# Kernel optimization log

Hardware: AMD Instinct MI355X
Metric: run time of the kernel (lower is better)

The kernel has to match this reference:

```python
import jax, jax.numpy as jnp
import numpy as np

D_MODEL = 1024
NUM_HEADS = 16
D_K = D_MODEL // NUM_HEADS


def setup_inputs() -> dict:
    key = jax.random.key(0)
    ks = jax.random.split(key, 9)
    B, S = 4, 2048
    scale = 1.0 / np.sqrt(D_MODEL)
    return {
        "hidden_states": jax.random.normal(ks[0], (B, S, D_MODEL), dtype=jnp.float32),
        "Wq": jax.random.normal(ks[1], (D_MODEL, D_MODEL), dtype=jnp.float32) * scale,
        "bq": jax.random.normal(ks[2], (D_MODEL,), dtype=jnp.float32) * 0.02,
        "Wk": jax.random.normal(ks[3], (D_MODEL, D_MODEL), dtype=jnp.float32) * scale,
        "bk": jax.random.normal(ks[4], (D_MODEL,), dtype=jnp.float32) * 0.02,
        "Wv": jax.random.normal(ks[5], (D_MODEL, D_MODEL), dtype=jnp.float32) * scale,
        "bv": jax.random.normal(ks[6], (D_MODEL,), dtype=jnp.float32) * 0.02,
        "Wout": jax.random.normal(ks[7], (D_MODEL, D_MODEL), dtype=jnp.float32) * scale,
        "bout": jax.random.normal(ks[8], (D_MODEL,), dtype=jnp.float32) * 0.02,
    }


def _split_heads(x):
    # [B, S, D] -> [B, H, S, d_k]
    B, S, _ = x.shape
    return x.reshape(B, S, NUM_HEADS, D_K).transpose(0, 2, 1, 3)


def reference(hidden_states, Wq, bq, Wk, bk, Wv, bv, Wout, bout):
    # torch nn.Linear convention: y = x @ W.T + b
    q = _split_heads(hidden_states @ Wq.T + bq)
    k = _split_heads(hidden_states @ Wk.T + bk)
    v = _split_heads(hidden_states @ Wv.T + bv)
    # scaled dot-product attention (no mask, matching attention_mask=None)
    scores = jnp.einsum("bhqd,bhkd->bhqk", q, k) / jnp.sqrt(jnp.float32(D_K))
    attn = jax.nn.softmax(scores, axis=-1)
    ctx = jnp.einsum("bhqk,bhkd->bhqd", attn, v)
    # concatenate heads: [B, H, S, d_k] -> [B, S, D]
    B, H, S, dk = ctx.shape
    ctx = ctx.transpose(0, 2, 1, 3).reshape(B, S, H * dk)
    return ctx @ Wout.T + bout
```

## Files before the change

### kernel.cpp

```cpp
#include <hip/hip_runtime.h>
#include <hip/hip_bf16.h>
#include <stdint.h>

#define DEV_INLINE __device__ __forceinline__

typedef __attribute__((ext_vector_type(4))) float f32x4;
typedef __attribute__((ext_vector_type(16))) float f32x16;
typedef __attribute__((ext_vector_type(8))) short short8;

static constexpr int S_LEN = 2048;
static constexpr int DM = 1024;
static constexpr int NH = 16;
static constexpr int DK = 64;
static constexpr int BATCH = 4;
static constexpr int M_TOT = BATCH * S_LEN;

#define QSCALE 0.18033688011112042f

DEV_INLINE unsigned short bf_round(float x) {
  unsigned u = __builtin_bit_cast(unsigned, x);
  u += 0x7fffu + ((u >> 16) & 1u);
  return (unsigned short)(u >> 16);
}

struct CvtArgs {
  const float* in[5];
  unsigned short* out[5];
};
__global__ __launch_bounds__(256) void cvt_all(CvtArgs a) {
  int bid = blockIdx.x;
  int which, base;
  if (bid < 4096) { which = 0; base = bid; }
  else { int r = bid - 4096; which = 1 + (r >> 9); base = r & 511; }
  const float* __restrict__ in = a.in[which];
  unsigned short* __restrict__ out = a.out[which];
  long i = ((long)base * 256 + threadIdx.x) * 8;
  float4 va = *reinterpret_cast<const float4*>(in + i);
  float4 vb = *reinterpret_cast<const float4*>(in + i + 4);
  union { unsigned short u[8]; uint4 v; } pk;
  pk.u[0] = bf_round(va.x); pk.u[1] = bf_round(va.y);
  pk.u[2] = bf_round(va.z); pk.u[3] = bf_round(va.w);
  pk.u[4] = bf_round(vb.x); pk.u[5] = bf_round(vb.y);
  pk.u[6] = bf_round(vb.z); pk.u[7] = bf_round(vb.w);
  *reinterpret_cast<uint4*>(out + i) = pk.v;
}

DEV_INLINE void gload_lds16(const unsigned short* g, unsigned short* l) {
  __builtin_amdgcn_global_load_lds(
      (const __attribute__((address_space(1))) unsigned int*)g,
      (__attribute__((address_space(3))) unsigned int*)l,
      16, 0, 0);
}

struct QkvArgs {
  const unsigned short* W[3];
  const float* bias[3];
  unsigned short* out[3];
};
__global__ __launch_bounds__(256) void gemm_qkv(const unsigned short* __restrict__ A,
                                                QkvArgs args) {
  constexpr int K = DM;
  __shared__ unsigned short lA[128 * 32];
  __shared__ unsigned short lB[128 * 32];
  const int tid = threadIdx.x;
  const int wave = tid >> 6, lane = tid & 63;
  const int wm = wave >> 1, wn = wave & 1;
  const int g = lane >> 4, c = lane & 15;
  const int bm = blockIdx.x, bn = blockIdx.y, z = blockIdx.z;

  const unsigned short* __restrict__ W = args.W[z];
  const float* __restrict__ bias = args.bias[z];
  unsigned short* __restrict__ outp = args.out[z];

  const int srow = lane >> 2;
  const int scol = (lane & 3) * 8;

  f32x4 acc[4][4] = {};

  const unsigned short* Abase = A + (long)(bm * 128) * K;
  const unsigned short* Wbase = W + (long)(bn * 128) * K;

  for (int k0 = 0; k0 < K; k0 += 32) {
    __syncthreads();
#pragma unroll
    for (int i = 0; i < 2; ++i) {
      const int row = i * 64 + wave * 16;
      gload_lds16(Abase + (long)(row + srow) * K + k0 + scol, lA + row * 32);
      gload_lds16(Wbase + (long)(row + srow) * K + k0 + scol, lB + row * 32);
    }
    __syncthreads();

    short8 af[4], bf[4];
#pragma unroll
    for (int mi = 0; mi < 4; ++mi)
      af[mi] = *reinterpret_cast<const short8*>(&lA[(wm * 64 + mi * 16 + c) * 32 + g * 8]);
#pragma unroll
    for (int ni = 0; ni < 4; ++ni)
      bf[ni] = *reinterpret_cast<const short8*>(&lB[(wn * 64 + ni * 16 + c) * 32 + g * 8]);
#pragma unroll
    for (int mi = 0; mi < 4; ++mi)
#pragma unroll
      for (int ni = 0; ni < 4; ++ni)
        acc[mi][ni] =
            __builtin_amdgcn_mfma_f32_16x16x32_bf16(af[mi], bf[ni], acc[mi][ni], 0, 0, 0);
  }

#pragma unroll
  for (int mi = 0; mi < 4; ++mi) {
#pragma unroll
    for (int ni = 0; ni < 4; ++ni) {
      const int mg0 = bm * 128 + wm * 64 + mi * 16 + g * 4;
      const int ng = bn * 128 + wn * 64 + ni * 16 + c;
      const float bv = bias[ng];
#pragma unroll
      for (int r = 0; r < 4; ++r) {
        const int m = mg0 + r;
        float v = acc[mi][ni][r] + bv;
        if (z == 0) v *= QSCALE;
        const int b_ = m >> 11, s_ = m & 2047, h_ = ng >> 6, d_ = ng & 63;
        if (z < 2) {
          outp[((long)(b_ * NH + h_) * S_LEN + s_) * DK + d_] = bf_round(v);
        } else {
          outp[((long)(b_ * NH + h_) * DK + d_) * S_LEN + s_] = bf_round(v);
        }
      }
    }
  }
}

__global__ __launch_bounds__(256) void gemm_out(const unsigned short* __restrict__ A,
                                                const unsigned short* __restrict__ W,
                                                const float* __restrict__ bias,
                                                float* __restrict__ outp) {
  constexpr int K = DM, N = DM;
  __shared__ unsigned short lA[128 * 32];
  __shared__ unsigned short lB[128 * 32];
  const int tid = threadIdx.x;
  const int wave = tid >> 6, lane = tid & 63;
  const int wm = wave >> 1, wn = wave & 1;
  const int g = lane >> 4, c = lane & 15;
  const int bm = blockIdx.x, bn = blockIdx.y;

  const int srow = lane >> 2;
  const int scol = (lane & 3) * 8;

  f32x4 acc[4][4] = {};

  const unsigned short* Abase = A + (long)(bm * 128) * K;
  const unsigned short* Wbase = W + (long)(bn * 128) * K;

  for (int k0 = 0; k0 < K; k0 += 32) {
    __syncthreads();
#pragma unroll
    for (int i = 0; i < 2; ++i) {
      const int row = i * 64 + wave * 16;
      gload_lds16(Abase + (long)(row + srow) * K + k0 + scol, lA + row * 32);
      gload_lds16(Wbase + (long)(row + srow) * K + k0 + scol, lB + row * 32);
    }
    __syncthreads();

    short8 af[4], bf[4];
#pragma unroll
    for (int mi = 0; mi < 4; ++mi)
      af[mi] = *reinterpret_cast<const short8*>(&lA[(wm * 64 + mi * 16 + c) * 32 + g * 8]);
#pragma unroll
    for (int ni = 0; ni < 4; ++ni)
      bf[ni] = *reinterpret_cast<const short8*>(&lB[(wn * 64 + ni * 16 + c) * 32 + g * 8]);
#pragma unroll
    for (int mi = 0; mi < 4; ++mi)
#pragma unroll
      for (int ni = 0; ni < 4; ++ni)
        acc[mi][ni] =
            __builtin_amdgcn_mfma_f32_16x16x32_bf16(af[mi], bf[ni], acc[mi][ni], 0, 0, 0);
  }

#pragma unroll
  for (int mi = 0; mi < 4; ++mi) {
#pragma unroll
    for (int ni = 0; ni < 4; ++ni) {
      const int mg0 = bm * 128 + wm * 64 + mi * 16 + g * 4;
      const int ng = bn * 128 + wn * 64 + ni * 16 + c;
      const float bv = bias[ng];
#pragma unroll
      for (int r = 0; r < 4; ++r)
        outp[(long)(mg0 + r) * N + ng] = acc[mi][ni][r] + bv;
    }
  }
}

__global__ __launch_bounds__(256) void attn_kernel(const unsigned short* __restrict__ Q,
                                                   const unsigned short* __restrict__ Kb,
                                                   const unsigned short* __restrict__ Vt,
                                                   unsigned short* __restrict__ ctx) {
  __shared__ unsigned short kbuf[2][64 * 64];
  __shared__ unsigned short vbuf[2][64 * 64];
  const int tid = threadIdx.x, wave = tid >> 6, lane = tid & 63;
  const int q = lane & 31;
  const int h = lane >> 5;
  const int bid = blockIdx.x;
  const int swz = (bid & 7) * 128 + (bid >> 3);
  const int hd = swz >> 4, qb = swz & 15;
  const int q0 = qb * 128 + wave * 32;

  const unsigned short* Qh = Q + (long)hd * S_LEN * DK;
  const char* KhB = (const char*)(Kb + (long)hd * S_LEN * DK);
  const char* VhB = (const char*)(Vt + (long)hd * DK * S_LEN);

  const int srow_in = lane >> 3;
  const int scolb = ((lane & 7) * 16) ^ (srow_in << 4);

  auto ldsrd = [&](const unsigned short* buf, int row, int colbyte) -> short8 {
    return *reinterpret_cast<const short8*>(
        reinterpret_cast<const char*>(buf) + row * 128 + (colbyte ^ ((row & 7) << 4)));
  };

  auto stage = [&](int b, int kv0) {
#pragma unroll
    for (int r = 0; r < 2; ++r) {
      const int rowbase = (wave * 2 + r) * 8;
      const int row = rowbase + srow_in;
      gload_lds16((const unsigned short*)(KhB + (long)(kv0 + row) * 128 + scolb),
                  &kbuf[b][rowbase * 64]);
      gload_lds16((const unsigned short*)(VhB + (long)row * (S_LEN * 2) + kv0 * 2 + scolb),
                  &vbuf[b][rowbase * 64]);
    }
  };

  short8 qf[4];
#pragma unroll
  for (int d0 = 0; d0 < 4; ++d0)
    qf[d0] = *reinterpret_cast<const short8*>(&Qh[(long)(q0 + q) * DK + d0 * 16 + h * 8]);

  f32x16 cacc0 = {}, cacc1 = {};
  float mrun = -1e30f, lrun = 0.0f;

  stage(0, 0);
  __syncthreads();

  int cur = 0;
  for (int t = 0; t < S_LEN / 64; ++t) {
    if (t + 1 < S_LEN / 64) stage(cur ^ 1, (t + 1) * 64);

    const unsigned short* kb = kbuf[cur];
    const unsigned short* vb = vbuf[cur];

    short8 kfA[4], kfB[4];
#pragma unroll
    for (int d0 = 0; d0 < 4; ++d0) {
      kfA[d0] = ldsrd(kb, q, d0 * 32 + h * 16);
      kfB[d0] = ldsrd(kb, 32 + q, d0 * 32 + h * 16);
    }
    __builtin_amdgcn_s_setprio(1);
    f32x16 stA = {}, stB = {};
#pragma unroll
    for (int d0 = 0; d0 < 4; ++d0) {
      stA = __builtin_amdgcn_mfma_f32_32x32x16_bf16(kfA[d0], qf[d0], stA, 0, 0, 0);
      stB = __builtin_amdgcn_mfma_f32_32x32x16_bf16(kfB[d0], qf[d0], stB, 0, 0, 0);
    }
    __builtin_amdgcn_s_setprio(0);

    float t16[16];
#pragma unroll
    for (int r = 0; r < 16; ++r) t16[r] = fmaxf(stA[r], stB[r]);
#pragma unroll
    for (int r = 0; r < 8; ++r) t16[r] = fmaxf(t16[r], t16[r + 8]);
#pragma unroll
    for (int r = 0; r < 4; ++r) t16[r] = fmaxf(t16[r], t16[r + 4]);
    const float pml = fmaxf(fmaxf(t16[0], t16[1]), fmaxf(t16[2], t16[3]));

    if (__any(pml > mrun + 8.0f)) {
      const float pm = fmaxf(pml, __shfl_xor(pml, 32));
      const float mnew = fmaxf(mrun, pm);
      const float alpha = __builtin_amdgcn_exp2f(mrun - mnew);
      cacc0 *= alpha;
      cacc1 *= alpha;
      lrun *= alpha;
      mrun = mnew;
    }

#pragma unroll
    for (int r = 0; r < 16; ++r) {
      stA[r] = __builtin_amdgcn_exp2f(stA[r] - mrun);
      stB[r] = __builtin_amdgcn_exp2f(stB[r] - mrun);
    }
    float s16[16];
#pragma unroll
    for (int r = 0; r < 16; ++r) s16[r] = stA[r] + stB[r];
#pragma unroll
    for (int r = 0; r < 8; ++r) s16[r] = s16[r] + s16[r + 8];
#pragma unroll
    for (int r = 0; r < 4; ++r) s16[r] = s16[r] + s16[r + 4];
    lrun += (s16[0] + s16[1]) + (s16[2] + s16[3]);

    unsigned pAA[4], pAB[4], pBA[4], pBB[4];
#pragma unroll
    for (int rq = 0; rq < 4; ++rq) {
      asm("v_cvt_pk_bf16_f32 %0, %1, %2" : "=v"(pAA[rq]) : "v"(stA[4 * rq]), "v"(stA[4 * rq + 1]));
      asm("v_cvt_pk_bf16_f32 %0, %1, %2" : "=v"(pAB[rq]) : "v"(stA[4 * rq + 2]), "v"(stA[4 * rq + 3]));
      asm("v_cvt_pk_bf16_f32 %0, %1, %2" : "=v"(pBA[rq]) : "v"(stB[4 * rq]), "v"(stB[4 * rq + 1]));
      asm("v_cvt_pk_bf16_f32 %0, %1, %2" : "=v"(pBB[rq]) : "v"(stB[4 * rq + 2]), "v"(stB[4 * rq + 3]));
    }

    unsigned rA[4], rB[4];
#pragma unroll
    for (int s = 0; s < 4; ++s) {
      const unsigned a0 = (s < 2 ? pAA : pBA)[2 * (s & 1)];
      const unsigned a1 = (s < 2 ? pAA : pBA)[2 * (s & 1) + 1];
      const unsigned b0 = (s < 2 ? pAB : pBB)[2 * (s & 1)];
      const unsigned b1 = (s < 2 ? pAB : pBB)[2 * (s & 1) + 1];
      rA[s] = (unsigned)__shfl_xor((int)(h ? a0 : a1), 32);
      rB[s] = (unsigned)__shfl_xor((int)(h ? b0 : b1), 32);
    }
    short8 vf0[4], vf1[4];
#pragma unroll
    for (int s = 0; s < 4; ++s) {
      vf0[s] = ldsrd(vb, q, s * 32 + h * 16);
      vf1[s] = ldsrd(vb, 32 + q, s * 32 + h * 16);
    }
    __builtin_amdgcn_s_setprio(1);
#pragma unroll
    for (int s = 0; s < 4; ++s) {
      const unsigned a0 = (s < 2 ? pAA : pBA)[2 * (s & 1)];
      const unsigned a1 = (s < 2 ? pAA : pBA)[2 * (s & 1) + 1];
      const unsigned b0 = (s < 2 ? pAB : pBB)[2 * (s & 1)];
      const unsigned b1 = (s < 2 ? pAB : pBB)[2 * (s & 1) + 1];
      union { unsigned w[4]; short8 v; } pf;
      pf.w[0] = h ? rA[s] : a0;
      pf.w[1] = h ? rB[s] : b0;
      pf.w[2] = h ? a1 : rA[s];
      pf.w[3] = h ? b1 : rB[s];
      cacc0 = __builtin_amdgcn_mfma_f32_32x32x16_bf16(vf0[s], pf.v, cacc0, 0, 0, 0);
      cacc1 = __builtin_amdgcn_mfma_f32_32x32x16_bf16(vf1[s], pf.v, cacc1, 0, 0, 0);
    }
    __builtin_amdgcn_s_setprio(0);

    __syncthreads();
    cur ^= 1;
  }

  lrun += __shfl_xor(lrun, 32);
  const float inv = 1.0f / lrun;
  const int b_ = hd >> 4, h_ = hd & 15;
  const long row = ((long)b_ * S_LEN + q0 + q) * DM + h_ * DK;
#pragma unroll
  for (int rq = 0; rq < 4; ++rq) {
    ushort4 w0, w1;
    w0.x = bf_round(cacc0[4 * rq + 0] * inv);
    w0.y = bf_round(cacc0[4 * rq + 1] * inv);
    w0.z = bf_round(cacc0[4 * rq + 2] * inv);
    w0.w = bf_round(cacc0[4 * rq + 3] * inv);
    w1.x = bf_round(cacc1[4 * rq + 0] * inv);
    w1.y = bf_round(cacc1[4 * rq + 1] * inv);
    w1.z = bf_round(cacc1[4 * rq + 2] * inv);
    w1.w = bf_round(cacc1[4 * rq + 3] * inv);
    *reinterpret_cast<ushort4*>(&ctx[row + 8 * rq + 4 * h]) = w0;
    *reinterpret_cast<ushort4*>(&ctx[row + 32 + 8 * rq + 4 * h]) = w1;
  }
}

extern "C" void kernel_launch(void* const* d_in, const int* in_sizes, int n_in,
                              void* d_out, int out_size, void* d_ws, size_t ws_size,
                              hipStream_t stream) {
  const float* X  = (const float*)d_in[0];
  const float* Wq = (const float*)d_in[1];
  const float* bq = (const float*)d_in[2];
  const float* Wk = (const float*)d_in[3];
  const float* bk = (const float*)d_in[4];
  const float* Wv = (const float*)d_in[5];
  const float* bv = (const float*)d_in[6];
  const float* Wo = (const float*)d_in[7];
  const float* bo = (const float*)d_in[8];

  char* ws = (char*)d_ws;
  const long MB = 1l << 20;
  unsigned short* Xbf = (unsigned short*)(ws + 0 * MB);
  unsigned short* Ctx = Xbf;
  unsigned short* Wqb = (unsigned short*)(ws + 16 * MB);
  unsigned short* Wkb = (unsigned short*)(ws + 18 * MB);
  unsigned short* Wvb = (unsigned short*)(ws + 20 * MB);
  unsigned short* Wob = (unsigned short*)(ws + 22 * MB);
  unsigned short* Qb  = (unsigned short*)(ws + 24 * MB);
  unsigned short* Kbf = (unsigned short*)(ws + 40 * MB);
  unsigned short* Vtb = (unsigned short*)(ws + 56 * MB);

  CvtArgs ca;
  ca.in[0] = X;  ca.out[0] = Xbf;
  ca.in[1] = Wq; ca.out[1] = Wqb;
  ca.in[2] = Wk; ca.out[2] = Wkb;
  ca.in[3] = Wv; ca.out[3] = Wvb;
  ca.in[4] = Wo; ca.out[4] = Wob;
  cvt_all<<<4096 + 4 * 512, 256, 0, stream>>>(ca);

  QkvArgs qa;
  qa.W[0] = Wqb; qa.bias[0] = bq; qa.out[0] = Qb;
  qa.W[1] = Wkb; qa.bias[1] = bk; qa.out[1] = Kbf;
  qa.W[2] = Wvb; qa.bias[2] = bv; qa.out[2] = Vtb;
  gemm_qkv<<<dim3(M_TOT / 128, DM / 128, 3), 256, 0, stream>>>(Xbf, qa);

  attn_kernel<<<dim3(1024), 256, 0, stream>>>(Qb, Kbf, Vtb, Ctx);

  gemm_out<<<dim3(M_TOT / 128, DM / 128), 256, 0, stream>>>(Ctx, Wob, bo, (float*)d_out);
}
```

Baseline: 227.7 us.

## Process two 32-row query tiles per wave in attention to reuse K/V fragments

Each wave now handles 64 query rows instead of 32, so every block covers 256 queries and the grid shrinks from 1024 to 512 blocks. K and V fragments read from LDS are reused across two independent query tiles, halving LDS reads and global K/V staging per query. The cost is roughly doubled accumulator and score register pressure, which may lower occupancy, and the smaller grid may leave compute units underused (512 blocks on a 256-CU device).

Measured after the change: 257.5 us. +13.1%, slower.

```diff
diff --git a/kernel.cpp b/kernel.cpp
--- a/kernel.cpp
+++ b/kernel.cpp
@@ -198,9 +198,9 @@
   const int q = lane & 31;
   const int h = lane >> 5;
   const int bid = blockIdx.x;
-  const int swz = (bid & 7) * 128 + (bid >> 3);
-  const int hd = swz >> 4, qb = swz & 15;
-  const int q0 = qb * 128 + wave * 32;
+  const int swz = (bid & 7) * 64 + (bid >> 3);
+  const int hd = swz >> 3, qb = swz & 7;
+  const int q0 = qb * 256 + wave * 64;
 
   const unsigned short* Qh = Q + (long)hd * S_LEN * DK;
   const char* KhB = (const char*)(Kb + (long)hd * S_LEN * DK);
@@ -226,13 +226,16 @@
     }
   };
 
-  short8 qf[4];
-#pragma unroll
-  for (int d0 = 0; d0 < 4; ++d0)
-    qf[d0] = *reinterpret_cast<const short8*>(&Qh[(long)(q0 + q) * DK + d0 * 16 + h * 8]);
-
-  f32x16 cacc0 = {}, cacc1 = {};
-  float mrun = -1e30f, lrun = 0.0f;
+  short8 qf0[4], qf1[4];
+#pragma unroll
+  for (int d0 = 0; d0 < 4; ++d0) {
+    qf0[d0] = *reinterpret_cast<const short8*>(&Qh[(long)(q0 + q) * DK + d0 * 16 + h * 8]);
+    qf1[d0] = *reinterpret_cast<const short8*>(&Qh[(long)(q0 + 32 + q) * DK + d0 * 16 + h * 8]);
+  }
+
+  f32x16 c00 = {}, c01 = {};
+  f32x16 c10 = {}, c11 = {};
+  float m0 = -1e30f, l0 = 0.0f, m1 = -1e30f, l1 = 0.0f;
 
   stage(0, 0);
   __syncthreads();
@@ -251,65 +254,82 @@
       kfB[d0] = ldsrd(kb, 32 + q, d0 * 32 + h * 16);
     }
     __builtin_amdgcn_s_setprio(1);
-    f32x16 stA = {}, stB = {};
+    f32x16 sA0 = {}, sB0 = {}, sA1 = {}, sB1 = {};
 #pragma unroll
     for (int d0 = 0; d0 < 4; ++d0) {
-      stA = __builtin_amdgcn_mfma_f32_32x32x16_bf16(kfA[d0], qf[d0], stA, 0, 0, 0);
-      stB = __builtin_amdgcn_mfma_f32_32x32x16_bf16(kfB[d0], qf[d0], stB, 0, 0, 0);
+      sA0 = __builtin_amdgcn_mfma_f32_32x32x16_bf16(kfA[d0], qf0[d0], sA0, 0, 0, 0);
+      sB0 = __builtin_amdgcn_mfma_f32_32x32x16_bf16(kfB[d0], qf0[d0], sB0, 0, 0, 0);
+      sA1 = __builtin_amdgcn_mfma_f32_32x32x16_bf16(kfA[d0], qf1[d0], sA1, 0, 0, 0);
+      sB1 = __builtin_amdgcn_mfma_f32_32x32x16_bf16(kfB[d0], qf1[d0], sB1, 0, 0, 0);
     }
     __builtin_amdgcn_s_setprio(0);
 
-    float t16[16];
-#pragma unroll
-    for (int r = 0; r < 16; ++r) t16[r] = fmaxf(stA[r], stB[r]);
-#pragma unroll
-    for (int r = 0; r < 8; ++r) t16[r] = fmaxf(t16[r], t16[r + 8]);
-#pragma unroll
-    for (int r = 0; r < 4; ++r) t16[r] = fmaxf(t16[r], t16[r + 4]);
-    const float pml = fmaxf(fmaxf(t16[0], t16[1]), fmaxf(t16[2], t16[3]));
-
-    if (__any(pml > mrun + 8.0f)) {
-      const float pm = fmaxf(pml, __shfl_xor(pml, 32));
-      const float mnew = fmaxf(mrun, pm);
-      const float alpha = __builtin_amdgcn_exp2f(mrun - mnew);
-      cacc0 *= alpha;
-      cacc1 *= alpha;
-      lrun *= alpha;
-      mrun = mnew;
+    float t0[16], t1[16];
+#pragma unroll
+    for (int r = 0; r < 16; ++r) { t0[r] = fmaxf(sA0[r], sB0[r]); t1[r] = fmaxf(sA1[r], sB1[r]); }
+#pragma unroll
+    for (int r = 0; r < 8; ++r) { t0[r] = fmaxf(t0[r], t0[r + 8]); t1[r] = fmaxf(t1[r], t1[r + 8]); }
+#pragma unroll
+    for (int r = 0; r < 4; ++r) { t0[r] = fmaxf(t0[r], t0[r + 4]); t1[r] = fmaxf(t1[r], t1[r + 4]); }
+    const float pml0 = fmaxf(fmaxf(t0[0], t0[1]), fmaxf(t0[2], t0[3]));
+    const float pml1 = fmaxf(fmaxf(t1[0], t1[1]), fmaxf(t1[2], t1[3]));
+
+    if (__any(fmaxf(pml0 - m0, pml1 - m1) > 8.0f)) {
+      const float pm0 = fmaxf(pml0, __shfl_xor(pml0, 32));
+      const float pm1 = fmaxf(pml1, __shfl_xor(pml1, 32));
+      const float mn0 = fmaxf(m0, pm0), mn1 = fmaxf(m1, pm1);
+      const float a0 = __builtin_amdgcn_exp2f(m0 - mn0);
+      const float a1 = __builtin_amdgcn_exp2f(m1 - mn1);
+      c00 *= a0; c01 *= a0; l0 *= a0; m0 = mn0;
+      c10 *= a1; c11 *= a1; l1 *= a1; m1 = mn1;
     }
 
 #pragma unroll
     for (int r = 0; r < 16; ++r) {
-      stA[r] = __builtin_amdgcn_exp2f(stA[r] - mrun);
-      stB[r] = __builtin_amdgcn_exp2f(stB[r] - mrun);
-    }
-    float s16[16];
-#pragma unroll
-    for (int r = 0; r < 16; ++r) s16[r] = stA[r] + stB[r];
-#pragma unroll
-    for (int r = 0; r < 8; ++r) s16[r] = s16[r] + s16[r + 8];
-#pragma unroll
-    for (int r = 0; r < 4; ++r) s16[r] = s16[r] + s16[r + 4];
-    lrun += (s16[0] + s16[1]) + (s16[2] + s16[3]);
-
-    unsigned pAA[4], pAB[4], pBA[4], pBB[4];
+      sA0[r] = __builtin_amdgcn_exp2f(sA0[r] - m0);
+      sB0[r] = __builtin_amdgcn_exp2f(sB0[r] - m0);
+      sA1[r] = __builtin_amdgcn_exp2f(sA1[r] - m1);
+      sB1[r] = __builtin_amdgcn_exp2f(sB1[r] - m1);
+    }
+    float u0[16], u1[16];
+#pragma unroll
+    for (int r = 0; r < 16; ++r) { u0[r] = sA0[r] + sB0[r]; u1[r] = sA1[r] + sB1[r]; }
+#pragma unroll
+    for (int r = 0; r < 8; ++r) { u0[r] += u0[r + 8]; u1[r] += u1[r + 8]; }
+#pragma unroll
+    for (int r = 0; r < 4; ++r) { u0[r] += u0[r + 4]; u1[r] += u1[r + 4]; }
+    l0 += (u0[0] + u0[1]) + (u0[2] + u0[3]);
+    l1 += (u1[0] + u1[1]) + (u1[2] + u1[3]);
+
+    unsigned p0AA[4], p0AB[4], p0BA[4], p0BB[4];
+    unsigned p1AA[4], p1AB[4], p1BA[4], p1BB[4];
 #pragma unroll
     for (int rq = 0; rq < 4; ++rq) {
-      asm("v_cvt_pk_bf16_f32 %0, %1, %2" : "=v"(pAA[rq]) : "v"(stA[4 * rq]), "v"(stA[4 * rq + 1]));
-      asm("v_cvt_pk_bf16_f32 %0, %1, %2" : "=v"(pAB[rq]) : "v"(stA[4 * rq + 2]), "v"(stA[4 * rq + 3]));
-      asm("v_cvt_pk_bf16_f32 %0, %1, %2" : "=v"(pBA[rq]) : "v"(stB[4 * rq]), "v"(stB[4 * rq + 1]));
-      asm("v_cvt_pk_bf16_f32 %0, %1, %2" : "=v"(pBB[rq]) : "v"(stB[4 * rq + 2]), "v"(stB[4 * rq + 3]));
-    }
-
-    unsigned rA[4], rB[4];
+      asm("v_cvt_pk_bf16_f32 %0, %1, %2" : "=v"(p0AA[rq]) : "v"(sA0[4 * rq]), "v"(sA0[4 * rq + 1]));
+      asm("v_cvt_pk_bf16_f32 %0, %1, %2" : "=v"(p0AB[rq]) : "v"(sA0[4 * rq + 2]), "v"(sA0[4 * rq + 3]));
+      asm("v_cvt_pk_bf16_f32 %0, %1, %2" : "=v"(p0BA[rq]) : "v"(sB0[4 * rq]), "v"(sB0[4 * rq + 1]));
+      asm("v_cvt_pk_bf16_f32 %0, %1, %2" : "=v"(p0BB[rq]) : "v"(sB0[4 * rq + 2]), "v"(sB0[4 * rq + 3]));
+      asm("v_cvt_pk_bf16_f32 %0, %1, %2" : "=v"(p1AA[rq]) : "v"(sA1[4 * rq]), "v"(sA1[4 * rq + 1]));
+      asm("v_cvt_pk_bf16_f32 %0, %1, %2" : "=v"(p1AB[rq]) : "v"(sA1[4 * rq + 2]), "v"(sA1[4 * rq + 3]));
+      asm("v_cvt_pk_bf16_f32 %0, %1, %2" : "=v"(p1BA[rq]) : "v"(sB1[4 * rq]), "v"(sB1[4 * rq + 1]));
+      asm("v_cvt_pk_bf16_f32 %0, %1, %2" : "=v"(p1BB[rq]) : "v"(sB1[4 * rq + 2]), "v"(sB1[4 * rq + 3]));
+    }
+
+    unsigned r0A[4], r0B[4], r1A[4], r1B[4];
 #pragma unroll
     for (int s = 0; s < 4; ++s) {
-      const unsigned a0 = (s < 2 ? pAA : pBA)[2 * (s & 1)];
-      const unsigned a1 = (s < 2 ? pAA : pBA)[2 * (s & 1) + 1];
-      const unsigned b0 = (s < 2 ? pAB : pBB)[2 * (s & 1)];
-      const unsigned b1 = (s < 2 ? pAB : pBB)[2 * (s & 1) + 1];
-      rA[s] = (unsigned)__shfl_xor((int)(h ? a0 : a1), 32);
-      rB[s] = (unsigned)__shfl_xor((int)(h ? b0 : b1), 32);
+      const unsigned a00 = (s < 2 ? p0AA : p0BA)[2 * (s & 1)];
+      const unsigned a01 = (s < 2 ? p0AA : p0BA)[2 * (s & 1) + 1];
+      const unsigned b00 = (s < 2 ? p0AB : p0BB)[2 * (s & 1)];
+      const unsigned b01 = (s < 2 ? p0AB : p0BB)[2 * (s & 1) + 1];
+      r0A[s] = (unsigned)__shfl_xor((int)(h ? a00 : a01), 32);
+      r0B[s] = (unsigned)__shfl_xor((int)(h ? b00 : b01), 32);
+      const unsigned a10 = (s < 2 ? p1AA : p1BA)[2 * (s & 1)];
+      const unsigned a11 = (s < 2 ? p1AA : p1BA)[2 * (s & 1) + 1];
+      const unsigned b10 = (s < 2 ? p1AB : p1BB)[2 * (s & 1)];
+      const unsigned b11 = (s < 2 ? p1AB : p1BB)[2 * (s & 1) + 1];
+      r1A[s] = (unsigned)__shfl_xor((int)(h ? a10 : a11), 32);
+      r1B[s] = (unsigned)__shfl_xor((int)(h ? b10 : b11), 32);
     }
     short8 vf0[4], vf1[4];
 #pragma unroll
@@ -320,17 +340,28 @@
     __builtin_amdgcn_s_setprio(1);
 #pragma unroll
     for (int s = 0; s < 4; ++s) {
-      const unsigned a0 = (s < 2 ? pAA : pBA)[2 * (s & 1)];
-      const unsigned a1 = (s < 2 ? pAA : pBA)[2 * (s & 1) + 1];
-      const unsigned b0 = (s < 2 ? pAB : pBB)[2 * (s & 1)];
-      const unsigned b1 = (s < 2 ? pAB : pBB)[2 * (s & 1) + 1];
-      union { unsigned w[4]; short8 v; } pf;
-      pf.w[0] = h ? rA[s] : a0;
-      pf.w[1] = h ? rB[s] : b0;
-      pf.w[2] = h ? a1 : rA[s];
-      pf.w[3] = h ? b1 : rB[s];
-      cacc0 = __builtin_amdgcn_mfma_f32_32x32x16_bf16(vf0[s], pf.v, cacc0, 0, 0, 0);
-      cacc1 = __builtin_amdgcn_mfma_f32_32x32x16_bf16(vf1[s], pf.v, cacc1, 0, 0, 0);
+      const unsigned a00 = (s < 2 ? p0AA : p0BA)[2 * (s & 1)];
+      const unsigned a01 = (s < 2 ? p0AA : p0BA)[2 * (s & 1) + 1];
+      const unsigned b00 = (s < 2 ? p0AB : p0BB)[2 * (s & 1)];
+      const unsigned b01 = (s < 2 ? p0AB : p0BB)[2 * (s & 1) + 1];
+      union { unsigned w[4]; short8 v; } pf0;
+      pf0.w[0] = h ? r0A[s] : a00;
+      pf0.w[1] = h ? r0B[s] : b00;
+      pf0.w[2] = h ? a01 : r0A[s];
+      pf0.w[3] = h ? b01 : r0B[s];
+      c00 = __builtin_amdgcn_mfma_f32_32x32x16_bf16(vf0[s], pf0.v, c00, 0, 0, 0);
+      c01 = __builtin_amdgcn_mfma_f32_32x32x16_bf16(vf1[s], pf0.v, c01, 0, 0, 0);
+      const unsigned a10 = (s < 2 ? p1AA : p1BA)[2 * (s & 1)];
+      const unsigned a11 = (s < 2 ? p1AA : p1BA)[2 * (s & 1) + 1];
+      const unsigned b10 = (s < 2 ? p1AB : p1BB)[2 * (s & 1)];
+      const unsigned b11 = (s < 2 ? p1AB : p1BB)[2 * (s & 1) + 1];
+      union { unsigned w[4]; short8 v; } pf1;
+      pf1.w[0] = h ? r1A[s] : a10;
+      pf1.w[1] = h ? r1B[s] : b10;
+      pf1.w[2] = h ? a11 : r1A[s];
+      pf1.w[3] = h ? b11 : r1B[s];
+      c10 = __builtin_amdgcn_mfma_f32_32x32x16_bf16(vf0[s], pf1.v, c10, 0, 0, 0);
+      c11 = __builtin_amdgcn_mfma_f32_32x32x16_bf16(vf1[s], pf1.v, c11, 0, 0, 0);
     }
     __builtin_amdgcn_s_setprio(0);
 
@@ -338,23 +369,35 @@
     cur ^= 1;
   }
 
-  lrun += __shfl_xor(lrun, 32);
-  const float inv = 1.0f / lrun;
+  l0 += __shfl_xor(l0, 32);
+  l1 += __shfl_xor(l1, 32);
+  const float inv0 = 1.0f / l0, inv1 = 1.0f / l1;
   const int b_ = hd >> 4, h_ = hd & 15;
-  const long row = ((long)b_ * S_LEN + q0 + q) * DM + h_ * DK;
+  const long row0 = ((long)b_ * S_LEN + q0 + q) * DM + h_ * DK;
+  const long row1 = ((long)b_ * S_LEN + q0 + 32 + q) * DM + h_ * DK;
 #pragma unroll
   for (int rq = 0; rq < 4; ++rq) {
-    ushort4 w0, w1;
-    w0.x = bf_round(cacc0[4 * rq + 0] * inv);
-    w0.y = bf_round(cacc0[4 * rq + 1] * inv);
-    w0.z = bf_round(cacc0[4 * rq + 2] * inv);
-    w0.w = bf_round(cacc0[4 * rq + 3] * inv);
-    w1.x = bf_round(cacc1[4 * rq + 0] * inv);
-    w1.y = bf_round(cacc1[4 * rq + 1] * inv);
-    w1.z = bf_round(cacc1[4 * rq + 2] * inv);
-    w1.w = bf_round(cacc1[4 * rq + 3] * inv);
-    *reinterpret_cast<ushort4*>(&ctx[row + 8 * rq + 4 * h]) = w0;
-    *reinterpret_cast<ushort4*>(&ctx[row + 32 + 8 * rq + 4 * h]) = w1;
+    ushort4 w0, w1, w2, w3;
+    w0.x = bf_round(c00[4 * rq + 0] * inv0);
+    w0.y = bf_round(c00[4 * rq + 1] * inv0);
+    w0.z = bf_round(c00[4 * rq + 2] * inv0);
+    w0.w = bf_round(c00[4 * rq + 3] * inv0);
+    w1.x = bf_round(c01[4 * rq + 0] * inv0);
+    w1.y = bf_round(c01[4 * rq + 1] * inv0);
+    w1.z = bf_round(c01[4 * rq + 2] * inv0);
+    w1.w = bf_round(c01[4 * rq + 3] * inv0);
+    w2.x = bf_round(c10[4 * rq + 0] * inv1);
+    w2.y = bf_round(c10[4 * rq + 1] * inv1);
+    w2.z = bf_round(c10[4 * rq + 2] * inv1);
+    w2.w = bf_round(c10[4 * rq + 3] * inv1);
+    w3.x = bf_round(c11[4 * rq + 0] * inv1);
+    w3.y = bf_round(c11[4 * rq + 1] * inv1);
+    w3.z = bf_round(c11[4 * rq + 2] * inv1);
+    w3.w = bf_round(c11[4 * rq + 3] * inv1);
+    *reinterpret_cast<ushort4*>(&ctx[row0 + 8 * rq + 4 * h]) = w0;
+    *reinterpret_cast<ushort4*>(&ctx[row0 + 32 + 8 * rq + 4 * h]) = w1;
+    *reinterpret_cast<ushort4*>(&ctx[row1 + 8 * rq + 4 * h]) = w2;
+    *reinterpret_cast<ushort4*>(&ctx[row1 + 32 + 8 * rq + 4 * h]) = w3;
   }
 }
 
@@ -397,7 +440,7 @@
   qa.W[2] = Wvb; qa.bias[2] = bv; qa.out[2] = Vtb;
   gemm_qkv<<<dim3(M_TOT / 128, DM / 128, 3), 256, 0, stream>>>(Xbf, qa);
 
-  attn_kernel<<<dim3(1024), 256, 0, stream>>>(Qb, Kbf, Vtb, Ctx);
+  attn_kernel<<<dim3(512), 256, 0, stream>>>(Qb, Kbf, Vtb, Ctx);
 
   gemm_out<<<dim3(M_TOT / 128, DM / 128), 256, 0, stream>>>(Ctx, Wob, bo, (float*)d_out);
 }
```

## Stage 128-key tiles per barrier and compute softmax row sums via MFMA

Applied to the files above, without the earlier changes.

The KV loop now stages two 64-row K/V sub-tiles per double-buffer slot, which halves the number of __syncthreads barriers and loads more data per prefetch. LDS use doubles to 64KB. The per-row softmax denominator is no longer a VALU reduction tree over fp32 probabilities. It is accumulated by an extra MFMA against a ones vector, using the bf16-rounded probabilities, which moves that work onto the matrix cores. The cost is 50% more MFMAs in the PV stage, possible occupancy loss from the larger LDS footprint, and a denominator computed from rounded values.

Result: no change. 226.5 us (-0.5%).

```diff
diff --git a/kernel.cpp b/kernel.cpp
--- a/kernel.cpp
+++ b/kernel.cpp
@@ -192,8 +192,8 @@
                                                    const unsigned short* __restrict__ Kb,
                                                    const unsigned short* __restrict__ Vt,
                                                    unsigned short* __restrict__ ctx) {
-  __shared__ unsigned short kbuf[2][64 * 64];
-  __shared__ unsigned short vbuf[2][64 * 64];
+  __shared__ unsigned short kbuf[2][2][64 * 64];
+  __shared__ unsigned short vbuf[2][2][64 * 64];
   const int tid = threadIdx.x, wave = tid >> 6, lane = tid & 63;
   const int q = lane & 31;
   const int h = lane >> 5;
@@ -216,13 +216,17 @@
 
   auto stage = [&](int b, int kv0) {
 #pragma unroll
-    for (int r = 0; r < 2; ++r) {
-      const int rowbase = (wave * 2 + r) * 8;
-      const int row = rowbase + srow_in;
-      gload_lds16((const unsigned short*)(KhB + (long)(kv0 + row) * 128 + scolb),
-                  &kbuf[b][rowbase * 64]);
-      gload_lds16((const unsigned short*)(VhB + (long)row * (S_LEN * 2) + kv0 * 2 + scolb),
-                  &vbuf[b][rowbase * 64]);
+    for (int sub = 0; sub < 2; ++sub) {
+#pragma unroll
+      for (int r = 0; r < 2; ++r) {
+        const int rowbase = (wave * 2 + r) * 8;
+        const int row = rowbase + srow_in;
+        gload_lds16((const unsigned short*)(KhB + (long)(kv0 + sub * 64 + row) * 128 + scolb),
+                    &kbuf[b][sub][rowbase * 64]);
+        gload_lds16((const unsigned short*)(VhB + (long)row * (S_LEN * 2) +
+                                            (kv0 + sub * 64) * 2 + scolb),
+                    &vbuf[b][sub][rowbase * 64]);
+      }
     }
   };
 
@@ -231,115 +235,116 @@
   for (int d0 = 0; d0 < 4; ++d0)
     qf[d0] = *reinterpret_cast<const short8*>(&Qh[(long)(q0 + q) * DK + d0 * 16 + h * 8]);
 
+  union { short s[8]; short8 v; } ones_u;
+#pragma unroll
+  for (int i = 0; i < 8; ++i) ones_u.s[i] = (short)0x3F80;
+  const short8 ones8 = ones_u.v;
+
   f32x16 cacc0 = {}, cacc1 = {};
-  float mrun = -1e30f, lrun = 0.0f;
+  f32x16 lacc = {};
+  float mrun = -1e30f;
 
   stage(0, 0);
   __syncthreads();
 
   int cur = 0;
-  for (int t = 0; t < S_LEN / 64; ++t) {
-    if (t + 1 < S_LEN / 64) stage(cur ^ 1, (t + 1) * 64);
-
-    const unsigned short* kb = kbuf[cur];
-    const unsigned short* vb = vbuf[cur];
-
-    short8 kfA[4], kfB[4];
-#pragma unroll
-    for (int d0 = 0; d0 < 4; ++d0) {
-      kfA[d0] = ldsrd(kb, q, d0 * 32 + h * 16);
-      kfB[d0] = ldsrd(kb, 32 + q, d0 * 32 + h * 16);
-    }
-    __builtin_amdgcn_s_setprio(1);
-    f32x16 stA = {}, stB = {};
-#pragma unroll
-    for (int d0 = 0; d0 < 4; ++d0) {
-      stA = __builtin_amdgcn_mfma_f32_32x32x16_bf16(kfA[d0], qf[d0], stA, 0, 0, 0);
-      stB = __builtin_amdgcn_mfma_f32_32x32x16_bf16(kfB[d0], qf[d0], stB, 0, 0, 0);
-    }
-    __builtin_amdgcn_s_setprio(0);
-
-    float t16[16];
-#pragma unroll
-    for (int r = 0; r < 16; ++r) t16[r] = fmaxf(stA[r], stB[r]);
-#pragma unroll
-    for (int r = 0; r < 8; ++r) t16[r] = fmaxf(t16[r], t16[r + 8]);
-#pragma unroll
-    for (int r = 0; r < 4; ++r) t16[r] = fmaxf(t16[r], t16[r + 4]);
-    const float pml = fmaxf(fmaxf(t16[0], t16[1]), fmaxf(t16[2], t16[3]));
-
-    if (__any(pml > mrun + 8.0f)) {
-      const float pm = fmaxf(pml, __shfl_xor(pml, 32));
-      const float mnew = fmaxf(mrun, pm);
-      const float alpha = __builtin_amdgcn_exp2f(mrun - mnew);
-      cacc0 *= alpha;
-      cacc1 *= alpha;
-      lrun *= alpha;
-      mrun = mnew;
-    }
-
-#pragma unroll
-    for (int r = 0; r < 16; ++r) {
-      stA[r] = __builtin_amdgcn_exp2f(stA[r] - mrun);
-      stB[r] = __builtin_amdgcn_exp2f(stB[r] - mrun);
-    }
-    float s16[16];
-#pragma unroll
-    for (int r = 0; r < 16; ++r) s16[r] = stA[r] + stB[r];
-#pragma unroll
-    for (int r = 0; r < 8; ++r) s16[r] = s16[r] + s16[r + 8];
-#pragma unroll
-    for (int r = 0; r < 4; ++r) s16[r] = s16[r] + s16[r + 4];
-    lrun += (s16[0] + s16[1]) + (s16[2] + s16[3]);
-
-    unsigned pAA[4], pAB[4], pBA[4], pBB[4];
-#pragma unroll
-    for (int rq = 0; rq < 4; ++rq) {
-      asm("v_cvt_pk_bf16_f32 %0, %1, %2" : "=v"(pAA[rq]) : "v"(stA[4 * rq]), "v"(stA[4 * rq + 1]));
-      asm("v_cvt_pk_bf16_f32 %0, %1, %2" : "=v"(pAB[rq]) : "v"(stA[4 * rq + 2]), "v"(stA[4 * rq + 3]));
-      asm("v_cvt_pk_bf16_f32 %0, %1, %2" : "=v"(pBA[rq]) : "v"(stB[4 * rq]), "v"(stB[4 * rq + 1]));
-      asm("v_cvt_pk_bf16_f32 %0, %1, %2" : "=v"(pBB[rq]) : "v"(stB[4 * rq + 2]), "v"(stB[4 * rq + 3]));
-    }
-
-    unsigned rA[4], rB[4];
-#pragma unroll
-    for (int s = 0; s < 4; ++s) {
-      const unsigned a0 = (s < 2 ? pAA : pBA)[2 * (s & 1)];
-      const unsigned a1 = (s < 2 ? pAA : pBA)[2 * (s & 1) + 1];
-      const unsigned b0 = (s < 2 ? pAB : pBB)[2 * (s & 1)];
-      const unsigned b1 = (s < 2 ? pAB : pBB)[2 * (s & 1) + 1];
-      rA[s] = (unsigned)__shfl_xor((int)(h ? a0 : a1), 32);
-      rB[s] = (unsigned)__shfl_xor((int)(h ? b0 : b1), 32);
-    }
-    short8 vf0[4], vf1[4];
-#pragma unroll
-    for (int s = 0; s < 4; ++s) {
-      vf0[s] = ldsrd(vb, q, s * 32 + h * 16);
-      vf1[s] = ldsrd(vb, 32 + q, s * 32 + h * 16);
-    }
-    __builtin_amdgcn_s_setprio(1);
-#pragma unroll
-    for (int s = 0; s < 4; ++s) {
-      const unsigned a0 = (s < 2 ? pAA : pBA)[2 * (s & 1)];
-      const unsigned a1 = (s < 2 ? pAA : pBA)[2 * (s & 1) + 1];
-      const unsigned b0 = (s < 2 ? pAB : pBB)[2 * (s & 1)];
-      const unsigned b1 = (s < 2 ? pAB : pBB)[2 * (s & 1) + 1];
-      union { unsigned w[4]; short8 v; } pf;
-      pf.w[0] = h ? rA[s] : a0;
-      pf.w[1] = h ? rB[s] : b0;
-      pf.w[2] = h ? a1 : rA[s];
-      pf.w[3] = h ? b1 : rB[s];
-      cacc0 = __builtin_amdgcn_mfma_f32_32x32x16_bf16(vf0[s], pf.v, cacc0, 0, 0, 0);
-      cacc1 = __builtin_amdgcn_mfma_f32_32x32x16_bf16(vf1[s], pf.v, cacc1, 0, 0, 0);
-    }
-    __builtin_amdgcn_s_setprio(0);
+  for (int t = 0; t < S_LEN / 128; ++t) {
+    if (t + 1 < S_LEN / 128) stage(cur ^ 1, (t + 1) * 128);
+
+#pragma unroll
+    for (int p = 0; p < 2; ++p) {
+      const unsigned short* kb = kbuf[cur][p];
+      const unsigned short* vb = vbuf[cur][p];
+
+      short8 kfA[4], kfB[4];
+#pragma unroll
+      for (int d0 = 0; d0 < 4; ++d0) {
+        kfA[d0] = ldsrd(kb, q, d0 * 32 + h * 16);
+        kfB[d0] = ldsrd(kb, 32 + q, d0 * 32 + h * 16);
+      }
+      __builtin_amdgcn_s_setprio(1);
+      f32x16 stA = {}, stB = {};
+#pragma unroll
+      for (int d0 = 0; d0 < 4; ++d0) {
+        stA = __builtin_amdgcn_mfma_f32_32x32x16_bf16(kfA[d0], qf[d0], stA, 0, 0, 0);
+        stB = __builtin_amdgcn_mfma_f32_32x32x16_bf16(kfB[d0], qf[d0], stB, 0, 0, 0);
+      }
+      __builtin_amdgcn_s_setprio(0);
+
+      float t16[16];
+#pragma unroll
+      for (int r = 0; r < 16; ++r) t16[r] = fmaxf(stA[r], stB[r]);
+#pragma unroll
+      for (int r = 0; r < 8; ++r) t16[r] = fmaxf(t16[r], t16[r + 8]);
+#pragma unroll
+      for (int r = 0; r < 4; ++r) t16[r] = fmaxf(t16[r], t16[r + 4]);
+      const float pml = fmaxf(fmaxf(t16[0], t16[1]), fmaxf(t16[2], t16[3]));
+
+      if (__any(pml > mrun + 8.0f)) {
+        const float pm = fmaxf(pml, __shfl_xor(pml, 32));
+        const float mnew = fmaxf(mrun, pm);
+        const float alpha = __builtin_amdgcn_exp2f(mrun - mnew);
+        cacc0 *= alpha;
+        cacc1 *= alpha;
+        lacc *= alpha;
+        mrun = mnew;
+      }
+
+#pragma unroll
+      for (int r = 0; r < 16; ++r) {
+        stA[r] = __builtin_amdgcn_exp2f(stA[r] - mrun);
+        stB[r] = __builtin_amdgcn_exp2f(stB[r] - mrun);
+      }
+
+      unsigned pAA[4], pAB[4], pBA[4], pBB[4];
+#pragma unroll
+      for (int rq = 0; rq < 4; ++rq) {
+        asm("v_cvt_pk_bf16_f32 %0, %1, %2" : "=v"(pAA[rq]) : "v"(stA[4 * rq]), "v"(stA[4 * rq + 1]));
+        asm("v_cvt_pk_bf16_f32 %0, %1, %2" : "=v"(pAB[rq]) : "v"(stA[4 * rq + 2]), "v"(stA[4 * rq + 3]));
+        asm("v_cvt_pk_bf16_f32 %0, %1, %2" : "=v"(pBA[rq]) : "v"(stB[4 * rq]), "v"(stB[4 * rq + 1]));
+        asm("v_cvt_pk_bf16_f32 %0, %1, %2" : "=v"(pBB[rq]) : "v"(stB[4 * rq + 2]), "v"(stB[4 * rq + 3]));
+      }
+
+      unsigned rA[4], rB[4];
+#pragma unroll
+      for (int s = 0; s < 4; ++s) {
+        const unsigned a0 = (s < 2 ? pAA : pBA)[2 * (s & 1)];
+        const unsigned a1 = (s < 2 ? pAA : pBA)[2 * (s & 1) + 1];
+        const unsigned b0 = (s < 2 ? pAB : pBB)[2 * (s & 1)];
+        const unsigned b1 = (s < 2 ? pAB : pBB)[2 * (s & 1) + 1];
+        rA[s] = (unsigned)__shfl_xor((int)(h ? a0 : a1), 32);
+        rB[s] = (unsigned)__shfl_xor((int)(h ? b0 : b1), 32);
+      }
+      short8 vf0[4], vf1[4];
+#pragma unroll
+      for (int s = 0; s < 4; ++s) {
+        vf0[s] = ldsrd(vb, q, s * 32 + h * 16);
+        vf1[s] = ldsrd(vb, 32 + q, s * 32 + h * 16);
+      }
+      __builtin_amdgcn_s_setprio(1);
+#pragma unroll
+      for (int s = 0; s < 4; ++s) {
+        const unsigned a0 = (s < 2 ? pAA : pBA)[2 * (s & 1)];
+        const unsigned a1 = (s < 2 ? pAA : pBA)[2 * (s & 1) + 1];
+        const unsigned b0 = (s < 2 ? pAB : pBB)[2 * (s & 1)];
+        const unsigned b1 = (s < 2 ? pAB : pBB)[2 * (s & 1) + 1];
+        union { unsigned w[4]; short8 v; } pf;
+        pf.w[0] = h ? rA[s] : a0;
+        pf.w[1] = h ? rB[s] : b0;
+        pf.w[2] = h ? a1 : rA[s];
+        pf.w[3] = h ? b1 : rB[s];
+        cacc0 = __builtin_amdgcn_mfma_f32_32x32x16_bf16(vf0[s], pf.v, cacc0, 0, 0, 0);
+        cacc1 = __builtin_amdgcn_mfma_f32_32x32x16_bf16(vf1[s], pf.v, cacc1, 0, 0, 0);
+        lacc = __builtin_amdgcn_mfma_f32_32x32x16_bf16(ones8, pf.v, lacc, 0, 0, 0);
+      }
+      __builtin_amdgcn_s_setprio(0);
+    }
 
     __syncthreads();
     cur ^= 1;
   }
 
-  lrun += __shfl_xor(lrun, 32);
-  const float inv = 1.0f / lrun;
+  const float inv = 1.0f / lacc[0];
   const int b_ = hd >> 4, h_ = hd & 15;
   const long row = ((long)b_ * S_LEN + q0 + q) * DM + h_ * DK;
 #pragma unroll
```
